# Optimization experiments

Hardware: AMD Instinct MI355X
Metric: run time of the kernel (lower is better)

Reference implementation:

```python
import jax, jax.numpy as jnp
import numpy as np

EPS = 1e-5
B, D_ENT, D_REL = 1024, 400, 400
OUT, KW = 32, 9
N_ENT = 50000


def _bn(x, g, b, axes):
    # batch-norm with batch statistics (training-mode math), eps=1e-5
    mu = jnp.mean(x, axis=axes, keepdims=True)
    var = jnp.var(x, axis=axes, keepdims=True)
    return (x - mu) * jax.lax.rsqrt(var + EPS) * g + b


def setup_inputs() -> dict:
    key = jax.random.key(0)
    ks = jax.random.split(key, 6)
    return {
        "e1_emb": jax.random.normal(ks[0], (B, D_ENT), jnp.float32),
        "rel_emb": jax.random.normal(ks[1], (B, D_REL), jnp.float32),
        "all_ent_w": jax.random.normal(ks[2], (N_ENT, D_ENT), jnp.float32),
        "fc1_w": jax.random.normal(ks[3], (OUT * KW, D_REL), jnp.float32) * 0.05,
        "fc1_b": jnp.zeros((OUT * KW,), jnp.float32),
        "fc_w": jax.random.normal(ks[4], (D_ENT, (D_ENT - KW + 1) * OUT), jnp.float32) * 0.02,
        "fc_b": jnp.zeros((D_ENT,), jnp.float32),
        "bn0_g": jnp.ones((1,), jnp.float32),
        "bn0_b": jnp.zeros((1,), jnp.float32),
        "bn1_g": jnp.ones((OUT,), jnp.float32),
        "bn1_b": jnp.zeros((OUT,), jnp.float32),
        "bn2_g": jnp.ones((D_ENT,), jnp.float32),
        "bn2_b": jnp.zeros((D_ENT,), jnp.float32),
    }


def reference(e1_emb, rel_emb, all_ent_w, fc1_w, fc1_b, fc_w, fc_b,
              bn0_g, bn0_b, bn1_g, bn1_b, bn2_g, bn2_b):
    d = e1_emb.shape[1]
    L = d - KW + 1  # conv output width (kernel_h=1, in_channels=1)

    # bn0: BatchNorm2d(1) over view [B,1,1,d] -> stats over all elements
    x = _bn(e1_emb, bn0_g, bn0_b, axes=(0, 1))  # [B, d]

    # hypernetwork: relation -> per-sample conv kernels [B, OUT, KW]
    k = (rel_emb @ fc1_w.T + fc1_b).reshape(-1, OUT, KW)

    # per-sample 1x9 conv (groups=B) as windows + batched contraction
    # xw[b, l, w] = x[b, l + w]
    xw = jnp.stack([x[:, w:w + L] for w in range(KW)], axis=-1)  # [B, L, KW]
    conv = jnp.einsum('blw,bow->bol', xw, k)  # [B, OUT, L]

    # bn1: BatchNorm2d(OUT), per-channel stats over (batch, width)
    h = _bn(conv, bn1_g[None, :, None], bn1_b[None, :, None], axes=(0, 2))

    # flatten channel-major (matches torch .view(B, -1) on [B, OUT, 1, L])
    h = h.reshape(h.shape[0], OUT * L)
    h = h @ fc_w.T + fc_b  # [B, d]

    # bn2: BatchNorm1d(d), per-feature stats over batch
    h = jax.nn.relu(_bn(h, bn2_g, bn2_b, axes=(0,)))

    return h @ all_ent_w.T  # [B, N_ENT]
```

## Files before the change

kernel.cpp:

```cpp
#include <hip/hip_runtime.h>
#include <stdint.h>

typedef unsigned short u16;
typedef short bf16x8 __attribute__((ext_vector_type(8)));
typedef float f32x4 __attribute__((ext_vector_type(4)));
typedef u16 u16x4 __attribute__((ext_vector_type(4)));
typedef u16 u16x8 __attribute__((ext_vector_type(8)));

#define B_SZ   1024
#define D_IN   400
#define L_OUT  392
#define OC     32
#define KW     9
#define K_FC   12544
#define N_ENT  50000
#define NPAD_ENT 50048
#define KPAD_H 448
#define NPAD_FC 512

__device__ __forceinline__ u16 f2bf(float f) {
  uint32_t u = __builtin_bit_cast(uint32_t, f);
  u += 0x7FFFu + ((u >> 16) & 1u);
  return (u16)(u >> 16);
}
__device__ __forceinline__ float bf2f(u16 v) {
  uint32_t u = ((uint32_t)v) << 16;
  return __builtin_bit_cast(float, u);
}

__device__ __forceinline__ void gload_lds16(const u16* g, u16* l) {
  __builtin_amdgcn_global_load_lds(
      (const __attribute__((address_space(1))) unsigned int*)g,
      (__attribute__((address_space(3))) unsigned int*)l, 16, 0, 0);
}

__device__ __forceinline__ void block_reduce2(float& s1, float& s2, float* sm) {
  for (int d = 32; d; d >>= 1) { s1 += __shfl_down(s1, d); s2 += __shfl_down(s2, d); }
  int wave = threadIdx.x >> 6, lane = threadIdx.x & 63;
  if (lane == 0) { sm[wave * 2] = s1; sm[wave * 2 + 1] = s2; }
  __syncthreads();
  if (threadIdx.x == 0) {
    s1 = sm[0] + sm[2] + sm[4] + sm[6];
    s2 = sm[1] + sm[3] + sm[5] + sm[7];
  }
}

__global__ __launch_bounds__(256) void red0(const float* __restrict__ e1, float* __restrict__ part0) {
  int t = threadIdx.x;
  int idx = blockIdx.x * 256 + t;
  float s1 = 0.f, s2 = 0.f;
  for (int i = idx; i < B_SZ * D_IN; i += 256 * 256) { float v = e1[i]; s1 += v; s2 += v * v; }
  __shared__ float sm[8];
  block_reduce2(s1, s2, sm);
  if (t == 0) { part0[blockIdx.x * 2] = s1; part0[blockIdx.x * 2 + 1] = s2; }
}

__global__ __launch_bounds__(256) void comb0(const float* __restrict__ part0,
                                             const float* __restrict__ g0,
                                             const float* __restrict__ b0,
                                             float* __restrict__ stats) {
  int t = threadIdx.x;
  float s1 = part0[t * 2], s2 = part0[t * 2 + 1];
  __shared__ float sm[8];
  block_reduce2(s1, s2, sm);
  if (t == 0) {
    const float N = (float)(B_SZ * D_IN);
    float mu = s1 / N, var = s2 / N - mu * mu;
    float a = g0[0] * rsqrtf(var + 1e-5f);
    stats[0] = a;
    stats[1] = b0[0] - mu * a;
  }
}

__global__ __launch_bounds__(256) void fc1_gemm(const float* __restrict__ rel,
                                                const float* __restrict__ W,
                                                const float* __restrict__ bias,
                                                float* __restrict__ outk) {
  __shared__ __align__(16) float As[16 * 68];
  __shared__ __align__(16) float Bs[16 * 68];
  int mt = blockIdx.x, nt = blockIdx.y;
  int t = threadIdx.x;
  int tx = t & 15, ty = t >> 4;
  int lr = t >> 2, lk = (t & 3) * 4;
  float acc[4][4] = {};
  for (int k0 = 0; k0 < 400; k0 += 16) {
    __syncthreads();
    float4 av = *(const float4*)(rel + (size_t)(mt * 64 + lr) * 400 + k0 + lk);
    int brow = nt * 64 + lr;
    float4 bv = {0.f, 0.f, 0.f, 0.f};
    if (brow < 288) bv = *(const float4*)(W + (size_t)brow * 400 + k0 + lk);
    As[(lk + 0) * 68 + lr] = av.x; As[(lk + 1) * 68 + lr] = av.y;
    As[(lk + 2) * 68 + lr] = av.z; As[(lk + 3) * 68 + lr] = av.w;
    Bs[(lk + 0) * 68 + lr] = bv.x; Bs[(lk + 1) * 68 + lr] = bv.y;
    Bs[(lk + 2) * 68 + lr] = bv.z; Bs[(lk + 3) * 68 + lr] = bv.w;
    __syncthreads();
#pragma unroll
    for (int k = 0; k < 16; ++k) {
      float4 a = *(const float4*)(As + k * 68 + ty * 4);
      float4 b = *(const float4*)(Bs + k * 68 + tx * 4);
      float aa[4] = {a.x, a.y, a.z, a.w}, bb[4] = {b.x, b.y, b.z, b.w};
#pragma unroll
      for (int i = 0; i < 4; ++i)
#pragma unroll
        for (int j = 0; j < 4; ++j) acc[i][j] += aa[i] * bb[j];
    }
  }
#pragma unroll
  for (int i = 0; i < 4; ++i) {
    int row = mt * 64 + ty * 4 + i;
#pragma unroll
    for (int j = 0; j < 4; ++j) {
      int col = nt * 64 + tx * 4 + j;
      if (col < 288) outk[(size_t)row * 288 + col] = acc[i][j] + bias[col];
    }
  }
}

__global__ __launch_bounds__(256) void conv_kernel(const float* __restrict__ e1,
                                                   const float* __restrict__ stats,
                                                   const float* __restrict__ kbuf,
                                                   u16* __restrict__ convA,
                                                   float* __restrict__ partial1) {
  int b = blockIdx.x, t = threadIdx.x;
  __shared__ __align__(16) float xs[D_IN];
  __shared__ float ks[OC * KW];
  float a0 = stats[0], b0c = stats[1];
  for (int i = t; i < D_IN; i += 256) xs[i] = e1[(size_t)b * D_IN + i] * a0 + b0c;
  for (int i = t; i < OC * KW; i += 256) ks[i] = kbuf[(size_t)b * (OC * KW) + i];
  __syncthreads();
  int o = t >> 3, sub = t & 7;
  float kw[KW];
#pragma unroll
  for (int w = 0; w < KW; ++w) kw[w] = ks[o * KW + w];
  float s1 = 0.f, s2 = 0.f;
  u16* orow = convA + (size_t)b * K_FC + o * L_OUT;
#pragma unroll
  for (int it = 0; it < 13; ++it) {
    int l = sub * 4 + it * 32;
    if (l < L_OUT) {
      float4 x0 = *(const float4*)(xs + l);
      float4 x1 = *(const float4*)(xs + l + 4);
      float4 x2 = *(const float4*)(xs + l + 8);
      float xv[12] = {x0.x, x0.y, x0.z, x0.w, x1.x, x1.y, x1.z, x1.w, x2.x, x2.y, x2.z, x2.w};
      u16x4 st;
#pragma unroll
      for (int j = 0; j < 4; ++j) {
        float c = 0.f;
#pragma unroll
        for (int w = 0; w < KW; ++w) c += xv[j + w] * kw[w];
        s1 += c; s2 += c * c;
        st[j] = f2bf(c);
      }
      *(u16x4*)(orow + l) = st;
    }
  }
  s1 += __shfl_down(s1, 4); s2 += __shfl_down(s2, 4);
  s1 += __shfl_down(s1, 2); s2 += __shfl_down(s2, 2);
  s1 += __shfl_down(s1, 1); s2 += __shfl_down(s2, 1);
  if (sub == 0) {
    partial1[b * 64 + o] = s1;
    partial1[b * 64 + 32 + o] = s2;
  }
}

__global__ __launch_bounds__(256) void comb1(const float* __restrict__ partial1,
                                             const float* __restrict__ g1,
                                             const float* __restrict__ b1,
                                             float* __restrict__ alphaK,
                                             float* __restrict__ betaK) {
  __shared__ float red[256];
  __shared__ float ab[64];
  int t = threadIdx.x;
  int s = t & 63, q = t >> 6;
  float acc = 0.f;
  for (int b = q * 256; b < q * 256 + 256; ++b) acc += partial1[b * 64 + s];
  red[t] = acc;
  __syncthreads();
  if (t < 64) red[t] = red[t] + red[t + 64] + red[t + 128] + red[t + 192];
  __syncthreads();
  if (t < 32) {
    const float N = (float)(B_SZ * L_OUT);
    float S1 = red[t], S2 = red[t + 32];
    float mu = S1 / N, var = S2 / N - mu * mu;
    float al = g1[t] * rsqrtf(var + 1e-5f);
    ab[t] = al;
    ab[32 + t] = b1[t] - mu * al;
  }
  __syncthreads();
  for (int i = t; i < K_FC; i += 256) {
    int o = i / L_OUT;
    alphaK[i] = ab[o];
    betaK[i] = ab[32 + o];
  }
}

__global__ __launch_bounds__(256) void bn1_apply(u16* __restrict__ convA,
                                                 const float* __restrict__ alphaK,
                                                 const float* __restrict__ betaK) {
  int gid = blockIdx.x * 256 + threadIdx.x;
  int row = gid / 1568, c = gid - row * 1568;
  int k = c * 8;
  u16* p = convA + (size_t)row * K_FC + k;
  u16x8 v = *(u16x8*)p;
  float4 a0 = *(const float4*)(alphaK + k);
  float4 a1 = *(const float4*)(alphaK + k + 4);
  float4 b0 = *(const float4*)(betaK + k);
  float4 b1 = *(const float4*)(betaK + k + 4);
  u16x8 o;
  o[0] = f2bf(bf2f(v[0]) * a0.x + b0.x);
  o[1] = f2bf(bf2f(v[1]) * a0.y + b0.y);
  o[2] = f2bf(bf2f(v[2]) * a0.z + b0.z);
  o[3] = f2bf(bf2f(v[3]) * a0.w + b0.w);
  o[4] = f2bf(bf2f(v[4]) * a1.x + b1.x);
  o[5] = f2bf(bf2f(v[5]) * a1.y + b1.y);
  o[6] = f2bf(bf2f(v[6]) * a1.z + b1.z);
  o[7] = f2bf(bf2f(v[7]) * a1.w + b1.w);
  *(u16x8*)p = o;
}

__global__ __launch_bounds__(256) void cvt_fcw(const float* __restrict__ src, u16* __restrict__ dst) {
  int gid = blockIdx.x * 256 + threadIdx.x;
  int row = gid / 1568, c = gid - row * 1568;
  int k = c * 8;
  u16x8 o = {};
  if (row < 400) {
    float4 f0 = *(const float4*)(src + (size_t)row * K_FC + k);
    float4 f1 = *(const float4*)(src + (size_t)row * K_FC + k + 4);
    o[0] = f2bf(f0.x); o[1] = f2bf(f0.y); o[2] = f2bf(f0.z); o[3] = f2bf(f0.w);
    o[4] = f2bf(f1.x); o[5] = f2bf(f1.y); o[6] = f2bf(f1.z); o[7] = f2bf(f1.w);
  }
  *(u16x8*)(dst + (size_t)row * K_FC + k) = o;
}

__global__ __launch_bounds__(256) void cvt_ent(const float* __restrict__ src, u16* __restrict__ dst) {
  int gid = blockIdx.x * 256 + threadIdx.x;
  int row = gid / 56, c = gid - row * 56;
  int k = c * 8;
  u16x8 o = {};
  if (row < N_ENT && k < D_IN) {
    float4 f0 = *(const float4*)(src + (size_t)row * D_IN + k);
    float4 f1 = *(const float4*)(src + (size_t)row * D_IN + k + 4);
    o[0] = f2bf(f0.x); o[1] = f2bf(f0.y); o[2] = f2bf(f0.z); o[3] = f2bf(f0.w);
    o[4] = f2bf(f1.x); o[5] = f2bf(f1.y); o[6] = f2bf(f1.z); o[7] = f2bf(f1.w);
  }
  *(u16x8*)(dst + (size_t)row * KPAD_H + k) = o;
}

__global__ __launch_bounds__(256) void bn2_kernel(const float* __restrict__ part2,
                                                  const float* __restrict__ g2,
                                                  const float* __restrict__ b2,
                                                  u16* __restrict__ hfin) {
  int j = blockIdx.x, t = threadIdx.x;
  if (j >= D_IN) {
    for (int b = t; b < B_SZ; b += 256) hfin[(size_t)b * KPAD_H + j] = 0;
    return;
  }
  float v[4], s1 = 0.f, s2 = 0.f;
#pragma unroll
  for (int i = 0; i < 4; ++i) {
    int b = t + i * 256;
    float acc = 0.f;
#pragma unroll
    for (int s = 0; s < 8; ++s) acc += part2[((size_t)s * B_SZ + b) * NPAD_FC + j];
    v[i] = acc; s1 += acc; s2 += acc * acc;
  }
  __shared__ float sm[8];
  block_reduce2(s1, s2, sm);
  __shared__ float albe[2];
  if (t == 0) {
    float mu = s1 / 1024.f, var = s2 / 1024.f - mu * mu;
    float al = g2[j] * rsqrtf(var + 1e-5f);
    albe[0] = al; albe[1] = b2[j] - mu * al;
  }
  __syncthreads();
  float al = albe[0], be = albe[1];
#pragma unroll
  for (int i = 0; i < 4; ++i) {
    float h = fmaxf(v[i] * al + be, 0.f);
    hfin[(size_t)(t + i * 256) * KPAD_H + j] = f2bf(h);
  }
}

__global__ __launch_bounds__(256) void gemm_bt(const u16* __restrict__ A,
                                               const u16* __restrict__ Bm,
                                               float* __restrict__ C,
                                               int Kpad, int mtiles, int ntiles,
                                               int ksteps_total, int ksteps_chunk,
                                               long ldc, int ncols_valid, long csplit_stride) {
  __shared__ __align__(16) u16 As[128 * 64];
  __shared__ __align__(16) u16 Bs[128 * 64];
  int bid = blockIdx.x;
  int mt = bid % mtiles;
  int nt = (bid / mtiles) % ntiles;
  int sp = bid / (mtiles * ntiles);
  int kbeg = sp * ksteps_chunk;
  int kend = kbeg + ksteps_chunk;
  if (kend > ksteps_total) kend = ksteps_total;

  int tid = threadIdx.x;
  int wave = tid >> 6, lane = tid & 63;
  int quad = lane >> 4, m16 = lane & 15;
  int rbase = (wave >> 1) * 64, cbase = (wave & 1) * 64;

  const u16* Arow0 = A + (size_t)mt * 128 * Kpad;
  const u16* Brow0 = Bm + (size_t)nt * 128 * Kpad;

  f32x4 acc[4][4] = {};

  for (int kt = kbeg; kt < kend; ++kt) {
    int k0 = kt * 64;
    __syncthreads();
#pragma unroll
    for (int p = 0; p < 4; ++p) {
      int slin = p * 256 + tid;
      int row = slin >> 3;
      int gch = (slin & 7) ^ (row & 7);
      u16* la = As + ((p * 256 + (wave << 6)) << 3);
      u16* lb = Bs + ((p * 256 + (wave << 6)) << 3);
      gload_lds16(Arow0 + (size_t)row * Kpad + k0 + gch * 8, la);
      gload_lds16(Brow0 + (size_t)row * Kpad + k0 + gch * 8, lb);
    }
    __syncthreads();
#pragma unroll
    for (int s = 0; s < 2; ++s) {
      bf16x8 af[4], bfr[4];
#pragma unroll
      for (int i = 0; i < 4; ++i) {
        int ar = rbase + i * 16 + m16;
        af[i] = *(const bf16x8*)(As + ar * 64 + (((s * 4 + quad) ^ (ar & 7)) << 3));
        int bc = cbase + i * 16 + m16;
        bfr[i] = *(const bf16x8*)(Bs + bc * 64 + (((s * 4 + quad) ^ (bc & 7)) << 3));
      }
#pragma unroll
      for (int i = 0; i < 4; ++i)
#pragma unroll
        for (int j = 0; j < 4; ++j)
          acc[i][j] = __builtin_amdgcn_mfma_f32_16x16x32_bf16(af[i], bfr[j], acc[i][j], 0, 0, 0);
    }
  }

  float* Cb = C + (size_t)sp * csplit_stride;
#pragma unroll
  for (int i = 0; i < 4; ++i) {
#pragma unroll
    for (int j = 0; j < 4; ++j) {
      int col = nt * 128 + cbase + j * 16 + m16;
      if (col < ncols_valid) {
        int row0 = mt * 128 + rbase + i * 16 + quad * 4;
#pragma unroll
        for (int r = 0; r < 4; ++r)
          Cb[(size_t)(row0 + r) * ldc + col] = acc[i][j][r];
      }
    }
  }
}

extern "C" void kernel_launch(void* const* d_in, const int* in_sizes, int n_in,
                              void* d_out, int out_size, void* d_ws, size_t ws_size,
                              hipStream_t stream) {
  const float* e1   = (const float*)d_in[0];
  const float* rel  = (const float*)d_in[1];
  const float* entw = (const float*)d_in[2];
  const float* fc1w = (const float*)d_in[3];
  const float* fc1b = (const float*)d_in[4];
  const float* fcw  = (const float*)d_in[5];
  const float* bn0g = (const float*)d_in[7];
  const float* bn0b = (const float*)d_in[8];
  const float* bn1g = (const float*)d_in[9];
  const float* bn1b = (const float*)d_in[10];
  const float* bn2g = (const float*)d_in[11];
  const float* bn2b = (const float*)d_in[12];
  float* out = (float*)d_out;

  char* ws = (char*)d_ws;
  size_t off = 0;
  auto alloc = [&](size_t bytes) -> void* {
    off = (off + 255) & ~(size_t)255;
    void* p = ws + off;
    off += bytes;
    return p;
  };
  float* stats    = (float*)alloc(16 * 4);
  float* part0    = (float*)alloc(512 * 4);
  float* kbuf     = (float*)alloc((size_t)B_SZ * 288 * 4);
  float* partial1 = (float*)alloc((size_t)B_SZ * 64 * 4);
  float* alphaK   = (float*)alloc((size_t)K_FC * 4);
  float* betaK    = (float*)alloc((size_t)K_FC * 4);
  u16*   convA    = (u16*)alloc((size_t)B_SZ * K_FC * 2);
  u16*   fcwb     = (u16*)alloc((size_t)NPAD_FC * K_FC * 2);
  float* part2    = (float*)alloc((size_t)8 * B_SZ * NPAD_FC * 4);
  u16*   hfin     = (u16*)alloc((size_t)B_SZ * KPAD_H * 2);
  u16*   entb     = (u16*)alloc((size_t)NPAD_ENT * KPAD_H * 2);

  red0<<<256, 256, 0, stream>>>(e1, part0);
  comb0<<<1, 256, 0, stream>>>(part0, bn0g, bn0b, stats);
  fc1_gemm<<<dim3(16, 5), 256, 0, stream>>>(rel, fc1w, fc1b, kbuf);
  conv_kernel<<<B_SZ, 256, 0, stream>>>(e1, stats, kbuf, convA, partial1);
  comb1<<<1, 256, 0, stream>>>(partial1, bn1g, bn1b, alphaK, betaK);
  bn1_apply<<<6272, 256, 0, stream>>>(convA, alphaK, betaK);
  cvt_fcw<<<3136, 256, 0, stream>>>(fcw, fcwb);
  gemm_bt<<<8 * 4 * 8, 256, 0, stream>>>(convA, fcwb, part2, K_FC, 8, 4, 196, 25,
                                         (long)NPAD_FC, NPAD_FC, (long)B_SZ * NPAD_FC);
  bn2_kernel<<<KPAD_H, 256, 0, stream>>>(part2, bn2g, bn2b, hfin);
  cvt_ent<<<10948, 256, 0, stream>>>(entw, entb);
  gemm_bt<<<8 * 391, 256, 0, stream>>>(hfin, entb, out, KPAD_H, 8, 391, 7, 7,
                                       (long)N_ENT, N_ENT, 0);
}
```

Before: 570.4 us.

## Fold BN1 scale into fc weights, widen split-K, retile bn2, swizzle entity GEMM

Removes the bn1_apply pass over the conv activations. The per-channel BN1 scale is folded into the bf16 conversion of fc_w. The BN1 shift is dropped on the grounds that it only adds a per-feature constant which BN2 then removes. The fc GEMM split-K grows from 8 to 14 chunks for more parallelism, and bn2 now handles 16 features per block with a 64-value register array. The final entity GEMM gets an XCD-aware block swizzle so blocks sharing an entity tile land on the same XCD for L2 reuse. The trade-offs are more partial-sum traffic, register pressure in bn2, and bf16 rounding of scaled weights.

Measured after the change: 555.4 us. 1.03x faster.

```diff
diff --git a/kernel.cpp b/kernel.cpp
--- a/kernel.cpp
+++ b/kernel.cpp
@@ -17,6 +17,7 @@
 #define NPAD_ENT 50048
 #define KPAD_H 448
 #define NPAD_FC 512
+#define SPLIT_FC 14
 
 __device__ __forceinline__ u16 f2bf(float f) {
   uint32_t u = __builtin_bit_cast(uint32_t, f);
@@ -165,11 +166,9 @@
 
 __global__ __launch_bounds__(256) void comb1(const float* __restrict__ partial1,
                                              const float* __restrict__ g1,
-                                             const float* __restrict__ b1,
-                                             float* __restrict__ alphaK,
-                                             float* __restrict__ betaK) {
+                                             float* __restrict__ alphaK) {
   __shared__ float red[256];
-  __shared__ float ab[64];
+  __shared__ float ab[32];
   int t = threadIdx.x;
   int s = t & 63, q = t >> 6;
   float acc = 0.f;
@@ -182,43 +181,18 @@
     const float N = (float)(B_SZ * L_OUT);
     float S1 = red[t], S2 = red[t + 32];
     float mu = S1 / N, var = S2 / N - mu * mu;
-    float al = g1[t] * rsqrtf(var + 1e-5f);
-    ab[t] = al;
-    ab[32 + t] = b1[t] - mu * al;
+    ab[t] = g1[t] * rsqrtf(var + 1e-5f);
   }
   __syncthreads();
   for (int i = t; i < K_FC; i += 256) {
     int o = i / L_OUT;
     alphaK[i] = ab[o];
-    betaK[i] = ab[32 + o];
-  }
-}
-
-__global__ __launch_bounds__(256) void bn1_apply(u16* __restrict__ convA,
-                                                 const float* __restrict__ alphaK,
-                                                 const float* __restrict__ betaK) {
-  int gid = blockIdx.x * 256 + threadIdx.x;
-  int row = gid / 1568, c = gid - row * 1568;
-  int k = c * 8;
-  u16* p = convA + (size_t)row * K_FC + k;
-  u16x8 v = *(u16x8*)p;
-  float4 a0 = *(const float4*)(alphaK + k);
-  float4 a1 = *(const float4*)(alphaK + k + 4);
-  float4 b0 = *(const float4*)(betaK + k);
-  float4 b1 = *(const float4*)(betaK + k + 4);
-  u16x8 o;
-  o[0] = f2bf(bf2f(v[0]) * a0.x + b0.x);
-  o[1] = f2bf(bf2f(v[1]) * a0.y + b0.y);
-  o[2] = f2bf(bf2f(v[2]) * a0.z + b0.z);
-  o[3] = f2bf(bf2f(v[3]) * a0.w + b0.w);
-  o[4] = f2bf(bf2f(v[4]) * a1.x + b1.x);
-  o[5] = f2bf(bf2f(v[5]) * a1.y + b1.y);
-  o[6] = f2bf(bf2f(v[6]) * a1.z + b1.z);
-  o[7] = f2bf(bf2f(v[7]) * a1.w + b1.w);
-  *(u16x8*)p = o;
-}
-
-__global__ __launch_bounds__(256) void cvt_fcw(const float* __restrict__ src, u16* __restrict__ dst) {
+  }
+}
+
+__global__ __launch_bounds__(256) void cvt_fcw(const float* __restrict__ src,
+                                               const float* __restrict__ alphaK,
+                                               u16* __restrict__ dst) {
   int gid = blockIdx.x * 256 + threadIdx.x;
   int row = gid / 1568, c = gid - row * 1568;
   int k = c * 8;
@@ -226,8 +200,12 @@
   if (row < 400) {
     float4 f0 = *(const float4*)(src + (size_t)row * K_FC + k);
     float4 f1 = *(const float4*)(src + (size_t)row * K_FC + k + 4);
-    o[0] = f2bf(f0.x); o[1] = f2bf(f0.y); o[2] = f2bf(f0.z); o[3] = f2bf(f0.w);
-    o[4] = f2bf(f1.x); o[5] = f2bf(f1.y); o[6] = f2bf(f1.z); o[7] = f2bf(f1.w);
+    float4 a0 = *(const float4*)(alphaK + k);
+    float4 a1 = *(const float4*)(alphaK + k + 4);
+    o[0] = f2bf(f0.x * a0.x); o[1] = f2bf(f0.y * a0.y);
+    o[2] = f2bf(f0.z * a0.z); o[3] = f2bf(f0.w * a0.w);
+    o[4] = f2bf(f1.x * a1.x); o[5] = f2bf(f1.y * a1.y);
+    o[6] = f2bf(f1.z * a1.z); o[7] = f2bf(f1.w * a1.w);
   }
   *(u16x8*)(dst + (size_t)row * K_FC + k) = o;
 }
@@ -250,34 +228,44 @@
                                                   const float* __restrict__ g2,
                                                   const float* __restrict__ b2,
                                                   u16* __restrict__ hfin) {
-  int j = blockIdx.x, t = threadIdx.x;
-  if (j >= D_IN) {
-    for (int b = t; b < B_SZ; b += 256) hfin[(size_t)b * KPAD_H + j] = 0;
-    return;
-  }
-  float v[4], s1 = 0.f, s2 = 0.f;
-#pragma unroll
-  for (int i = 0; i < 4; ++i) {
-    int b = t + i * 256;
+  int j0 = blockIdx.x * 16;
+  int t = threadIdx.x;
+  int tj = t & 15, tb = t >> 4;
+  int j = j0 + tj;
+  float v[64];
+  float s1 = 0.f, s2 = 0.f;
+#pragma unroll 2
+  for (int i = 0; i < 64; ++i) {
+    int b = tb + i * 16;
     float acc = 0.f;
 #pragma unroll
-    for (int s = 0; s < 8; ++s) acc += part2[((size_t)s * B_SZ + b) * NPAD_FC + j];
+    for (int s = 0; s < SPLIT_FC; ++s)
+      acc += part2[((size_t)s * B_SZ + b) * NPAD_FC + j];
     v[i] = acc; s1 += acc; s2 += acc * acc;
   }
-  __shared__ float sm[8];
-  block_reduce2(s1, s2, sm);
-  __shared__ float albe[2];
-  if (t == 0) {
-    float mu = s1 / 1024.f, var = s2 / 1024.f - mu * mu;
-    float al = g2[j] * rsqrtf(var + 1e-5f);
-    albe[0] = al; albe[1] = b2[j] - mu * al;
-  }
-  __syncthreads();
-  float al = albe[0], be = albe[1];
-#pragma unroll
-  for (int i = 0; i < 4; ++i) {
-    float h = fmaxf(v[i] * al + be, 0.f);
-    hfin[(size_t)(t + i * 256) * KPAD_H + j] = f2bf(h);
+  __shared__ float sm1[16][17], sm2[16][17];
+  sm1[tb][tj] = s1; sm2[tb][tj] = s2;
+  __syncthreads();
+  __shared__ float albe[2][16];
+  if (t < 16) {
+    float S1 = 0.f, S2 = 0.f;
+#pragma unroll
+    for (int r = 0; r < 16; ++r) { S1 += sm1[r][t]; S2 += sm2[r][t]; }
+    int jf = j0 + t;
+    float al = 0.f, be = 0.f;
+    if (jf < D_IN) {
+      float mu = S1 / 1024.f, var = S2 / 1024.f - mu * mu;
+      al = g2[jf] * rsqrtf(var + 1e-5f);
+      be = b2[jf] - mu * al;
+    }
+    albe[0][t] = al; albe[1][t] = be;
+  }
+  __syncthreads();
+  float al = albe[0][tj], be = albe[1][tj];
+#pragma unroll 2
+  for (int i = 0; i < 64; ++i) {
+    int b = tb + i * 16;
+    hfin[(size_t)b * KPAD_H + j] = f2bf(fmaxf(v[i] * al + be, 0.f));
   }
 }
 
@@ -286,13 +274,23 @@
                                                float* __restrict__ C,
                                                int Kpad, int mtiles, int ntiles,
                                                int ksteps_total, int ksteps_chunk,
-                                               long ldc, int ncols_valid, long csplit_stride) {
+                                               long ldc, int ncols_valid, long csplit_stride,
+                                               int xcd_swz) {
   __shared__ __align__(16) u16 As[128 * 64];
   __shared__ __align__(16) u16 Bs[128 * 64];
   int bid = blockIdx.x;
-  int mt = bid % mtiles;
-  int nt = (bid / mtiles) % ntiles;
-  int sp = bid / (mtiles * ntiles);
+  int mt, nt, sp;
+  if (xcd_swz) {
+    int r = bid & 7, g = bid >> 3;
+    mt = g & 7;
+    nt = (g >> 3) * 8 + r;
+    sp = 0;
+    if (nt >= ntiles) return;
+  } else {
+    mt = bid % mtiles;
+    nt = (bid / mtiles) % ntiles;
+    sp = bid / (mtiles * ntiles);
+  }
   int kbeg = sp * ksteps_chunk;
   int kend = kbeg + ksteps_chunk;
   if (kend > ksteps_total) kend = ksteps_total;
@@ -367,7 +365,6 @@
   const float* bn0g = (const float*)d_in[7];
   const float* bn0b = (const float*)d_in[8];
   const float* bn1g = (const float*)d_in[9];
-  const float* bn1b = (const float*)d_in[10];
   const float* bn2g = (const float*)d_in[11];
   const float* bn2b = (const float*)d_in[12];
   float* out = (float*)d_out;
@@ -385,10 +382,9 @@
   float* kbuf     = (float*)alloc((size_t)B_SZ * 288 * 4);
   float* partial1 = (float*)alloc((size_t)B_SZ * 64 * 4);
   float* alphaK   = (float*)alloc((size_t)K_FC * 4);
-  float* betaK    = (float*)alloc((size_t)K_FC * 4);
   u16*   convA    = (u16*)alloc((size_t)B_SZ * K_FC * 2);
   u16*   fcwb     = (u16*)alloc((size_t)NPAD_FC * K_FC * 2);
-  float* part2    = (float*)alloc((size_t)8 * B_SZ * NPAD_FC * 4);
+  float* part2    = (float*)alloc((size_t)SPLIT_FC * B_SZ * NPAD_FC * 4);
   u16*   hfin     = (u16*)alloc((size_t)B_SZ * KPAD_H * 2);
   u16*   entb     = (u16*)alloc((size_t)NPAD_ENT * KPAD_H * 2);
 
@@ -396,13 +392,12 @@
   comb0<<<1, 256, 0, stream>>>(part0, bn0g, bn0b, stats);
   fc1_gemm<<<dim3(16, 5), 256, 0, stream>>>(rel, fc1w, fc1b, kbuf);
   conv_kernel<<<B_SZ, 256, 0, stream>>>(e1, stats, kbuf, convA, partial1);
-  comb1<<<1, 256, 0, stream>>>(partial1, bn1g, bn1b, alphaK, betaK);
-  bn1_apply<<<6272, 256, 0, stream>>>(convA, alphaK, betaK);
-  cvt_fcw<<<3136, 256, 0, stream>>>(fcw, fcwb);
-  gemm_bt<<<8 * 4 * 8, 256, 0, stream>>>(convA, fcwb, part2, K_FC, 8, 4, 196, 25,
-                                         (long)NPAD_FC, NPAD_FC, (long)B_SZ * NPAD_FC);
-  bn2_kernel<<<KPAD_H, 256, 0, stream>>>(part2, bn2g, bn2b, hfin);
+  comb1<<<1, 256, 0, stream>>>(partial1, bn1g, alphaK);
+  cvt_fcw<<<3136, 256, 0, stream>>>(fcw, alphaK, fcwb);
+  gemm_bt<<<8 * 4 * SPLIT_FC, 256, 0, stream>>>(convA, fcwb, part2, K_FC, 8, 4, 196, 14,
+                                                (long)NPAD_FC, NPAD_FC, (long)B_SZ * NPAD_FC, 0);
+  bn2_kernel<<<KPAD_H / 16, 256, 0, stream>>>(part2, bn2g, bn2b, hfin);
   cvt_ent<<<10948, 256, 0, stream>>>(entw, entb);
-  gemm_bt<<<8 * 391, 256, 0, stream>>>(hfin, entb, out, KPAD_H, 8, 391, 7, 7,
-                                       (long)N_ENT, N_ENT, 0);
-}
+  gemm_bt<<<8 * 392, 256, 0, stream>>>(hfin, entb, out, KPAD_H, 8, 391, 7, 7,
+                                       (long)N_ENT, N_ENT, 0, 1);
+}
```
